# Kernel tuning notes

Hardware: AMD Instinct MI355X
Metric: run time of the kernel (lower is better)

The kernel has to match this reference:

```python
import jax, jax.numpy as jnp
import numpy as np

B = 64           # images
C = 100          # num_categories
LOOP = 3         # LOOP_NUM: max boxes per (image, category)
NB_PER = 150     # boxes per image
N = B * NB_PER   # total boxes
FEAT = 2052      # 2048 backbone feats + 4 bbox coords
OUT = 2048       # gcn_output_shape


def _occ_slots(key):
    """For each element, its occurrence index among equal-valued keys (stable order)."""
    n = key.shape[0]
    order = jnp.argsort(key, stable=True)
    sk = key[order]
    idx = jnp.arange(n)
    is_new = jnp.concatenate([jnp.ones((1,), bool), sk[1:] != sk[:-1]])
    run_start = jax.lax.cummax(jnp.where(is_new, idx, 0))
    pos = idx - run_start
    return jnp.zeros(n, dtype=jnp.int32).at[order].set(pos.astype(jnp.int32))


def setup_inputs() -> dict:
    key = jax.random.key(0)
    ks = jax.random.split(key, 8)
    image_features = jax.random.normal(ks[0], (N, 2048), jnp.float32)
    bbox_list = jax.random.uniform(ks[1], (N, 4), jnp.float32)
    global_features = jax.random.normal(ks[2], (B, C), jnp.float32)
    adj = jax.random.uniform(ks[3], (B, C, C), jnp.float32)
    X = jnp.full((C, C), 1e-6, jnp.float32)                 # nn.Parameter init
    lin_w = jax.random.normal(ks[4], (LOOP,), jnp.float32) * 0.5   # Linear(3,1) weight
    lin_b = jax.random.normal(ks[5], (), jnp.float32) * 0.1        # Linear(3,1) bias
    gc_w = jax.random.normal(ks[6], (FEAT, OUT), jnp.float32) / np.sqrt(FEAT)
    gc_b = jnp.zeros((OUT,), jnp.float32)
    # labels cycle 1..C so each (image, category) appears <= ceil(NB_PER/C)=2 <= LOOP times
    label_list = (jnp.arange(N, dtype=jnp.int32) % C) + 1
    batch = (jnp.arange(N, dtype=jnp.int32) // NB_PER)
    return dict(image_features=image_features, bbox_list=bbox_list,
                global_features=global_features, adj=adj, X=X,
                lin_w=lin_w, lin_b=lin_b, gc_w=gc_w, gc_b=gc_b,
                label_list=label_list, batch=batch)


def reference(image_features, bbox_list, global_features, adj, X,
              lin_w, lin_b, gc_w, gc_b, label_list, batch):
    # full_features = concat(backbone feats, bbox): [N, 2052]
    full = jnp.concatenate([image_features, bbox_list], axis=1)
    cat = label_list - 1
    # occurrence slot of each box within its (image, category) bucket
    slots = _occ_slots(batch.astype(jnp.int64) * C + cat.astype(jnp.int64))
    # scatter-build gcn_input: [B, C, LOOP, 2052]
    gcn_input = jnp.zeros((B, C, LOOP, FEAT), full.dtype).at[batch, cat, slots].set(full)
    # transpose(2,3) then Linear(LOOP -> 1) and squeeze: [B, C, 2052]
    x = jnp.einsum('bcld,l->bcd', gcn_input, lin_w) + lin_b
    # new_adj = X + adj; GraphConvolution: adj @ (x @ W) + b, then leaky_relu
    new_adj = X[None, :, :] + adj
    support = jnp.einsum('bcd,do->bco', x, gc_w)          # [B, C, 2048]
    gcn_out = jax.nn.leaky_relu(jnp.einsum('bcn,bno->bco', new_adj, support) + gc_b)
    # attention aggregate: [B,1,C] @ [B,C,OUT] -> [B,OUT]
    return jnp.einsum('bc,bco->bo', global_features, gcn_out)
```

## Files before the change

kernel.cpp:

```cpp
#include <hip/hip_runtime.h>
#include <stdint.h>

#define BB    64
#define CC    100
#define NBPER 150
#define FEAT  2052
#define KP    2112
#define NOUT  2048
#define MR    6400

typedef __attribute__((ext_vector_type(8))) short   short8;
typedef __attribute__((ext_vector_type(4))) float   floatx4;

__device__ __forceinline__ unsigned short f2bf(float f) {
  unsigned int u = __float_as_uint(f);
  u += 0x7FFFu + ((u >> 16) & 1u);
  return (unsigned short)(u >> 16);
}

__device__ __forceinline__ void async16(const void* g, void* l) {
  __builtin_amdgcn_global_load_lds((__attribute__((address_space(1))) void*)(g),
                                   (__attribute__((address_space(3))) void*)(l),
                                   16, 0, 0);
}

__global__ __launch_bounds__(256) void k_prep(const float* __restrict__ gcw,
                                              unsigned short* __restrict__ gcwT,
                                              const float* __restrict__ imgf,
                                              const float* __restrict__ bbox,
                                              const float* __restrict__ lw,
                                              const float* __restrict__ lb,
                                              const int* __restrict__ labels,
                                              unsigned short* __restrict__ xbf,
                                              const float* __restrict__ X,
                                              const float* __restrict__ adj,
                                              unsigned short* __restrict__ A2p) {
  __shared__ float smf[64 * 65];
  const int bx  = blockIdx.x;
  const int tid = threadIdx.x;

  if (bx < 768) {
    int*   lab  = (int*)smf;
    int*   sidx = lab + NBPER;
    float* swt  = (float*)(sidx + 3 * CC);
    const int bimg = bx / 12;
    const int sl   = bx - bimg * 12;
    if (tid < NBPER) lab[tid] = labels[bimg * NBPER + tid];
    __syncthreads();
    if (tid < CC) {
      int i0 = 0, i1 = 0, i2 = 0, cnt = 0;
      float w0 = 0.f, w1 = 0.f, w2 = 0.f;
      for (int i = 0; i < NBPER; ++i) {
        if (lab[i] == tid + 1) {
          if (cnt == 0)      { i0 = bimg * NBPER + i; w0 = lw[0]; }
          else if (cnt == 1) { i1 = bimg * NBPER + i; w1 = lw[1]; }
          else if (cnt == 2) { i2 = bimg * NBPER + i; w2 = lw[2]; }
          ++cnt;
        }
      }
      sidx[tid * 3] = i0; sidx[tid * 3 + 1] = i1; sidx[tid * 3 + 2] = i2;
      swt[tid * 3] = w0;  swt[tid * 3 + 1] = w1;  swt[tid * 3 + 2] = w2;
    }
    __syncthreads();
    const float bias = lb[0];
    for (int idx = tid; idx < CC * 22; idx += 256) {
      const int cl  = idx / 22;
      const int col = sl * 22 + (idx - cl * 22);
      const int d0  = col * 8;
      const int r   = bimg * CC + cl;
      const int i0 = sidx[cl * 3], i1 = sidx[cl * 3 + 1], i2 = sidx[cl * 3 + 2];
      const float w0 = swt[cl * 3], w1 = swt[cl * 3 + 1], w2 = swt[cl * 3 + 2];
      float v[8];
      if (d0 < 2048) {
        const float4* p0 = (const float4*)(imgf + (size_t)i0 * 2048 + d0);
        const float4* p1 = (const float4*)(imgf + (size_t)i1 * 2048 + d0);
        const float4* p2 = (const float4*)(imgf + (size_t)i2 * 2048 + d0);
        float4 a0 = p0[0], a1 = p0[1];
        float4 b0 = p1[0], b1 = p1[1];
        float4 c0 = p2[0], c1 = p2[1];
        v[0] = bias + w0 * a0.x + w1 * b0.x + w2 * c0.x;
        v[1] = bias + w0 * a0.y + w1 * b0.y + w2 * c0.y;
        v[2] = bias + w0 * a0.z + w1 * b0.z + w2 * c0.z;
        v[3] = bias + w0 * a0.w + w1 * b0.w + w2 * c0.w;
        v[4] = bias + w0 * a1.x + w1 * b1.x + w2 * c1.x;
        v[5] = bias + w0 * a1.y + w1 * b1.y + w2 * c1.y;
        v[6] = bias + w0 * a1.z + w1 * b1.z + w2 * c1.z;
        v[7] = bias + w0 * a1.w + w1 * b1.w + w2 * c1.w;
      } else if (d0 == 2048) {
        float4 u0 = *(const float4*)(bbox + (size_t)i0 * 4);
        float4 u1 = *(const float4*)(bbox + (size_t)i1 * 4);
        float4 u2 = *(const float4*)(bbox + (size_t)i2 * 4);
        v[0] = bias + w0 * u0.x + w1 * u1.x + w2 * u2.x;
        v[1] = bias + w0 * u0.y + w1 * u1.y + w2 * u2.y;
        v[2] = bias + w0 * u0.z + w1 * u1.z + w2 * u2.z;
        v[3] = bias + w0 * u0.w + w1 * u1.w + w2 * u2.w;
        v[4] = 0.f; v[5] = 0.f; v[6] = 0.f; v[7] = 0.f;
      } else {
#pragma unroll
        for (int q = 0; q < 8; ++q) v[q] = 0.f;
      }
      unsigned short o[8] __attribute__((aligned(16)));
#pragma unroll
      for (int q = 0; q < 8; ++q) o[q] = f2bf(v[q]);
      *(uint4*)(xbf + (size_t)r * KP + d0) = *(const uint4*)o;
    }
    return;
  }

  if (bx < 1824) {
    const int t  = bx - 768;
    const int ko = t % 33;
    const int oo = t / 33;
    const int cc = tid & 63, r0 = tid >> 6;
#pragma unroll
    for (int i = 0; i < 16; ++i) {
      const int r = r0 * 16 + i;
      const int k = ko * 64 + r;
      smf[r * 65 + cc] = (k < FEAT) ? gcw[(size_t)k * NOUT + oo * 64 + cc] : 0.f;
    }
    __syncthreads();
    const int ol = tid >> 2;
    const int kq = tid & 3;
    unsigned short buf[16] __attribute__((aligned(16)));
#pragma unroll
    for (int j = 0; j < 16; ++j) buf[j] = f2bf(smf[(kq * 16 + j) * 65 + ol]);
    const size_t base = (size_t)(oo * 64 + ol) * KP + ko * 64 + kq * 16;
    *(uint4*)&gcwT[base]     = *(const uint4*)&buf[0];
    *(uint4*)&gcwT[base + 8] = *(const uint4*)&buf[8];
    return;
  }

  {
    const int b = bx - 1824;
#pragma unroll
    for (int it = 0; it < 16; ++it) {
      const int idx = it * 256 + tid;
      const int c = idx >> 5, ng = idx & 31;
      const int n = ng * 4;
      unsigned short pk[4] __attribute__((aligned(8))) = {0, 0, 0, 0};
      if (c < CC && n < CC) {
        const float4 a4 = *(const float4*)(adj + (size_t)b * (CC * CC) + c * CC + n);
        const float4 x4 = *(const float4*)(X + c * CC + n);
        pk[0] = f2bf(a4.x + x4.x); pk[1] = f2bf(a4.y + x4.y);
        pk[2] = f2bf(a4.z + x4.z); pk[3] = f2bf(a4.w + x4.w);
      }
      *(uint2*)&A2p[((size_t)b * 128 + c) * 128 + n] = *(const uint2*)pk;
    }
  }
}

__global__ __launch_bounds__(256) void k_gemm1(const unsigned short* __restrict__ A,
                                               const unsigned short* __restrict__ Bt,
                                               unsigned short* __restrict__ ST) {
  __shared__ unsigned short shbuf[128 * 132] __attribute__((aligned(16)));
  unsigned short* Asm = shbuf;
  unsigned short* Bsm = shbuf + 8192;
  const int tid  = threadIdx.x;
  const int lane = tid & 63;
  const int w    = tid >> 6;
  const int v    = blockIdx.y * gridDim.x + blockIdx.x;
  const int ncol = (v & 7) * 2 + ((v >> 3) & 1);
  const int mrow = v >> 4;
  const int m0   = mrow * 128;
  const int n0   = ncol * 128;
  const int wm   = (w & 1) * 64;
  const int wn   = (w >> 1) * 64;
  const int srow = lane >> 3;
  const int gk   = (((lane & 7) - srow) & 7) * 8;
  const int quad = lane >> 4;
  const int lrow = lane & 15;
  const int rot  = (lane & 7) * 8;

  floatx4 acc[4][4] = {};

  for (int kb = 0; kb < KP / 64; ++kb) {
    const int k0 = kb * 64;
#pragma unroll
    for (int t = 0; t < 4; ++t) {
      const int chunk = t * 4 + w;
      const int row = chunk * 8 + srow;
      async16(A  + (size_t)(m0 + row) * KP + (k0 + gk), &Asm[chunk * 512]);
      async16(Bt + (size_t)(n0 + row) * KP + (k0 + gk), &Bsm[chunk * 512]);
    }
    __syncthreads();
#pragma unroll
    for (int kp = 0; kp < 2; ++kp) {
      const int koff = (kp * 32 + quad * 8 + rot) & 63;
      short8 af[4], bfr[4];
#pragma unroll
      for (int i = 0; i < 4; ++i)
        af[i]  = *(const short8*)&Asm[(wm + i * 16 + lrow) * 64 + koff];
#pragma unroll
      for (int j = 0; j < 4; ++j)
        bfr[j] = *(const short8*)&Bsm[(wn + j * 16 + lrow) * 64 + koff];
#pragma unroll
      for (int i = 0; i < 4; ++i)
#pragma unroll
        for (int j = 0; j < 4; ++j)
          acc[i][j] = __builtin_amdgcn_mfma_f32_16x16x32_bf16(af[i], bfr[j], acc[i][j], 0, 0, 0);
    }
    __syncthreads();
  }

#pragma unroll
  for (int j = 0; j < 4; ++j) {
    const int ol = wn + j * 16 + lrow;
#pragma unroll
    for (int i = 0; i < 4; ++i) {
#pragma unroll
      for (int rr = 0; rr < 4; ++rr) {
        const int ml = wm + i * 16 + quad * 4 + rr;
        shbuf[ol * 132 + ml] = f2bf(acc[i][j][rr]);
      }
    }
  }
  __syncthreads();
#pragma unroll
  for (int it = 0; it < 32; ++it) {
    const int idx = it * 256 + tid;
    const int o = idx >> 6;
    const int cp = idx & 63;
    const int m = 2 * cp;
    const int r = m0 + m;
    const int b = r / 100;
    const int c = r - b * 100;
    const unsigned int val = *(const unsigned int*)&shbuf[o * 132 + m];
    *(unsigned int*)&ST[((size_t)b * NOUT + n0 + o) * 128 + c] = val;
  }
}

__global__ __launch_bounds__(256) void k_gemm2(const unsigned short* __restrict__ A2p,
                                               const unsigned short* __restrict__ ST,
                                               const float* __restrict__ gf,
                                               const float* __restrict__ gcb,
                                               float* __restrict__ outp) {
  __shared__ unsigned short A2s[128 * 64] __attribute__((aligned(16)));
  __shared__ unsigned short Ssm[128 * 64] __attribute__((aligned(16)));
  __shared__ float gsm[128];
  __shared__ float red[128 * 9];
  const int tid = threadIdx.x;
  const int o0  = blockIdx.x * 128;
  const int b   = blockIdx.y;
  if (tid < 128) gsm[tid] = (tid < CC) ? gf[b * CC + tid] : 0.f;

  const int lane = tid & 63;
  const int w    = tid >> 6;
  const int srow = lane >> 3;
  const int gk   = (((lane & 7) - srow) & 7) * 8;
  const int quad = lane >> 4;
  const int lrow = lane & 15;
  const int rot  = (lane & 7) * 8;
  const int wm   = (w & 1) * 64;
  const int wn   = (w >> 1) * 64;

  floatx4 acc[4][4] = {};

  for (int kb = 0; kb < 2; ++kb) {
    const int k0 = kb * 64;
    __syncthreads();
#pragma unroll
    for (int t = 0; t < 4; ++t) {
      const int chunk = t * 4 + w;
      const int row = chunk * 8 + srow;
      async16(A2p + ((size_t)b * 128 + row) * 128 + k0 + gk, &A2s[chunk * 512]);
      async16(ST + ((size_t)b * NOUT + o0 + row) * 128 + k0 + gk, &Ssm[chunk * 512]);
    }
    __syncthreads();
#pragma unroll
    for (int kp = 0; kp < 2; ++kp) {
      const int koff = (kp * 32 + quad * 8 + rot) & 63;
      short8 af[4], bfr[4];
#pragma unroll
      for (int i = 0; i < 4; ++i)
        af[i]  = *(const short8*)&A2s[(wm + i * 16 + lrow) * 64 + koff];
#pragma unroll
      for (int j = 0; j < 4; ++j)
        bfr[j] = *(const short8*)&Ssm[(wn + j * 16 + lrow) * 64 + koff];
#pragma unroll
      for (int i = 0; i < 4; ++i)
#pragma unroll
        for (int j = 0; j < 4; ++j)
          acc[i][j] = __builtin_amdgcn_mfma_f32_16x16x32_bf16(af[i], bfr[j], acc[i][j], 0, 0, 0);
    }
  }
  __syncthreads();

  const int slot = (w & 1) * 4 + quad;
#pragma unroll
  for (int j = 0; j < 4; ++j) {
    const int ol = wn + j * 16 + lrow;
    const float bias = gcb[o0 + ol];
    float s = 0.f;
#pragma unroll
    for (int i = 0; i < 4; ++i) {
#pragma unroll
      for (int rr = 0; rr < 4; ++rr) {
        const int c = wm + i * 16 + quad * 4 + rr;
        float t = acc[i][j][rr] + bias;
        t = (t > 0.f) ? t : 0.01f * t;
        s += gsm[c] * t;
      }
    }
    red[ol * 9 + slot] = s;
  }
  __syncthreads();
  if (tid < 128) {
    float s = 0.f;
#pragma unroll
    for (int t = 0; t < 8; ++t) s += red[tid * 9 + t];
    outp[(size_t)b * NOUT + o0 + tid] = s;
  }
}

extern "C" void kernel_launch(void* const* d_in, const int* in_sizes, int n_in,
                              void* d_out, int out_size, void* d_ws, size_t ws_size,
                              hipStream_t stream) {
  const float* imgf   = (const float*)d_in[0];
  const float* bbox   = (const float*)d_in[1];
  const float* gfeat  = (const float*)d_in[2];
  const float* adj    = (const float*)d_in[3];
  const float* X      = (const float*)d_in[4];
  const float* lw     = (const float*)d_in[5];
  const float* lb     = (const float*)d_in[6];
  const float* gcw    = (const float*)d_in[7];
  const float* gcb    = (const float*)d_in[8];
  const int*   labels = (const int*)d_in[9];

  char* ws = (char*)d_ws;
  unsigned short* xbf      = (unsigned short*)(ws);
  unsigned short* gcwT     = (unsigned short*)(ws + 27033600);
  unsigned short* supportT = (unsigned short*)(ws + 35684352);
  unsigned short* A2p      = (unsigned short*)(ws + 69238784);
  float*          outp     = (float*)d_out;

  k_prep<<<dim3(1888), dim3(256), 0, stream>>>(gcw, gcwT, imgf, bbox, lw, lb,
                                               labels, xbf, X, adj, A2p);
  k_gemm1<<<dim3(16, 50), dim3(256), 0, stream>>>(xbf, gcwT, supportT);
  k_gemm2<<<dim3(NOUT / 128, BB), dim3(256), 0, stream>>>(A2p, supportT, gfeat, gcb, outp);
}
```

Baseline: 266.2 us.

## Rewrite support GEMM as 256x256-tile, 512-thread double-buffered pipelined kernel

The first GEMM now uses 256x256 output tiles per 512-thread block (8 waves, 128x64 per wave) instead of 128x128 tiles per 256 threads. Global-to-LDS async loads are double-buffered and interleaved with MFMA quarters using explicit vmcnt waits, barriers and s_setprio, so memory traffic overlaps compute rather than stalling on a full sync each k-step. The block-to-tile mapping is also remapped across 200 blocks. The design trades a larger register and LDS footprint and a hand-tuned barrier schedule for more operand reuse and better latency hiding. The epilogue is split into two halves so the transpose fits in the reused LDS.

```diff
diff --git a/kernel.cpp b/kernel.cpp
--- a/kernel.cpp
+++ b/kernel.cpp
@@ -149,83 +149,138 @@
   }
 }
 
-__global__ __launch_bounds__(256) void k_gemm1(const unsigned short* __restrict__ A,
-                                               const unsigned short* __restrict__ Bt,
-                                               unsigned short* __restrict__ ST) {
-  __shared__ unsigned short shbuf[128 * 132] __attribute__((aligned(16)));
-  unsigned short* Asm = shbuf;
-  unsigned short* Bsm = shbuf + 8192;
+__global__ __launch_bounds__(512, 2) void k_gemm1(const unsigned short* __restrict__ Ax,
+                                                  const unsigned short* __restrict__ Bx,
+                                                  unsigned short* __restrict__ ST) {
+  __shared__ unsigned short sh[2][2][16384] __attribute__((aligned(16)));
   const int tid  = threadIdx.x;
   const int lane = tid & 63;
   const int w    = tid >> 6;
-  const int v    = blockIdx.y * gridDim.x + blockIdx.x;
-  const int ncol = (v & 7) * 2 + ((v >> 3) & 1);
-  const int mrow = v >> 4;
-  const int m0   = mrow * 128;
-  const int n0   = ncol * 128;
-  const int wm   = (w & 1) * 64;
-  const int wn   = (w >> 1) * 64;
+  const int wr   = w >> 2;
+  const int wc   = w & 3;
   const int srow = lane >> 3;
   const int gk   = (((lane & 7) - srow) & 7) * 8;
   const int quad = lane >> 4;
   const int lrow = lane & 15;
   const int rot  = (lane & 7) * 8;
-
-  floatx4 acc[4][4] = {};
-
-  for (int kb = 0; kb < KP / 64; ++kb) {
-    const int k0 = kb * 64;
-#pragma unroll
-    for (int t = 0; t < 4; ++t) {
-      const int chunk = t * 4 + w;
-      const int row = chunk * 8 + srow;
-      async16(A  + (size_t)(m0 + row) * KP + (k0 + gk), &Asm[chunk * 512]);
-      async16(Bt + (size_t)(n0 + row) * KP + (k0 + gk), &Bsm[chunk * 512]);
-    }
-    __syncthreads();
-#pragma unroll
-    for (int kp = 0; kp < 2; ++kp) {
-      const int koff = (kp * 32 + quad * 8 + rot) & 63;
-      short8 af[4], bfr[4];
-#pragma unroll
-      for (int i = 0; i < 4; ++i)
-        af[i]  = *(const short8*)&Asm[(wm + i * 16 + lrow) * 64 + koff];
-#pragma unroll
-      for (int j = 0; j < 4; ++j)
-        bfr[j] = *(const short8*)&Bsm[(wn + j * 16 + lrow) * 64 + koff];
-#pragma unroll
-      for (int i = 0; i < 4; ++i)
-#pragma unroll
-        for (int j = 0; j < 4; ++j)
-          acc[i][j] = __builtin_amdgcn_mfma_f32_16x16x32_bf16(af[i], bfr[j], acc[i][j], 0, 0, 0);
-    }
-    __syncthreads();
-  }
-
-#pragma unroll
-  for (int j = 0; j < 4; ++j) {
-    const int ol = wn + j * 16 + lrow;
-#pragma unroll
-    for (int i = 0; i < 4; ++i) {
-#pragma unroll
-      for (int rr = 0; rr < 4; ++rr) {
-        const int ml = wm + i * 16 + quad * 4 + rr;
-        shbuf[ol * 132 + ml] = f2bf(acc[i][j][rr]);
-      }
-    }
-  }
+  const int v    = (blockIdx.x & 7) * 25 + (blockIdx.x >> 3);
+  const int ncol = v / 25;
+  const int mrow = v - ncol * 25;
+  const int m0   = mrow * 256;
+  const int n0   = ncol * 256;
+  const int wm   = wr * 128;
+  const int wn   = wc * 64;
+
+  const unsigned short* pA = Ax + (size_t)(m0 + w * 8 + srow) * KP + gk;
+  const unsigned short* pB = Bx + (size_t)(n0 + w * 8 + srow) * KP + gk;
+
+  floatx4 acc[8][4] = {};
+  short8  afrag[4][2], bfrag[4][2];
+
+#define STG_A(DB, HH, K0) do {                                            \
+    const unsigned short* s_ = pA + (size_t)((HH) * 128) * KP + (K0);     \
+    async16(s_,           &sh[DB][0][(HH) * 8192 + w * 512]);             \
+    async16(s_ + 64 * KP, &sh[DB][0][(HH) * 8192 + (8 + w) * 512]);       \
+  } while (0)
+#define STG_B(DB, HH, K0) do {                                            \
+    const unsigned short* s_ = pB + (size_t)((HH) * 128) * KP + (K0);     \
+    async16(s_,           &sh[DB][1][(HH) * 8192 + w * 512]);             \
+    async16(s_ + 64 * KP, &sh[DB][1][(HH) * 8192 + (8 + w) * 512]);       \
+  } while (0)
+#define RD_B(DB) do {                                                     \
+    _Pragma("unroll") for (int g = 0; g < 4; ++g)                         \
+    _Pragma("unroll") for (int kk = 0; kk < 2; ++kk)                      \
+      bfrag[g][kk] = *(const short8*)&sh[DB][1][(wn + g * 16 + lrow) * 64 \
+                                    + ((kk * 32 + quad * 8 + rot) & 63)]; \
+  } while (0)
+#define RD_A(DB, FO) do {                                                 \
+    _Pragma("unroll") for (int f = 0; f < 4; ++f)                         \
+    _Pragma("unroll") for (int kk = 0; kk < 2; ++kk)                      \
+      afrag[f][kk] = *(const short8*)&sh[DB][0][(wm + ((FO) + f) * 16 + lrow) * 64 \
+                                    + ((kk * 32 + quad * 8 + rot) & 63)]; \
+  } while (0)
+#define MFMA_Q(FO, GO) do {                                               \
+    __builtin_amdgcn_s_setprio(1);                                        \
+    _Pragma("unroll") for (int f = 0; f < 4; ++f)                         \
+    _Pragma("unroll") for (int g = 0; g < 2; ++g)                         \
+    _Pragma("unroll") for (int kk = 0; kk < 2; ++kk)                      \
+      acc[(FO) + f][(GO) + g] = __builtin_amdgcn_mfma_f32_16x16x32_bf16(  \
+          afrag[f][kk], bfrag[(GO) + g][kk], acc[(FO) + f][(GO) + g], 0, 0, 0); \
+    __builtin_amdgcn_s_setprio(0);                                        \
+  } while (0)
+#define BAR __builtin_amdgcn_s_barrier()
+#define VM6 asm volatile("s_waitcnt vmcnt(6)" ::: "memory")
+#define VM0 asm volatile("s_waitcnt vmcnt(0)" ::: "memory")
+
+  STG_B(0, 0, 0);  STG_B(0, 1, 0);  STG_A(0, 0, 0);  STG_A(0, 1, 0);
+  STG_B(1, 0, 64); STG_B(1, 1, 64); STG_A(1, 0, 64);
+  VM6; BAR;
+
+#pragma unroll 1
+  for (int i = 0; i < 15; ++i) {
+    const int kT1 = i * 128 + 64, kT2 = i * 128 + 128, kT3 = i * 128 + 192;
+    RD_B(0); RD_A(0, 0); STG_A(1, 1, kT1); BAR; MFMA_Q(0, 0); BAR;
+    STG_B(0, 0, kT2);                      BAR; MFMA_Q(0, 2); BAR;
+    RD_A(0, 4); STG_B(0, 1, kT2);          BAR; MFMA_Q(4, 0); BAR;
+    STG_A(0, 0, kT2);                      BAR; MFMA_Q(4, 2); VM6; BAR;
+    RD_B(1); RD_A(1, 0); STG_A(0, 1, kT2); BAR; MFMA_Q(0, 0); BAR;
+    STG_B(1, 0, kT3);                      BAR; MFMA_Q(0, 2); BAR;
+    RD_A(1, 4); STG_B(1, 1, kT3);          BAR; MFMA_Q(4, 0); BAR;
+    STG_A(1, 0, kT3);                      BAR; MFMA_Q(4, 2); VM6; BAR;
+  }
+  RD_B(0); RD_A(0, 0); STG_A(1, 1, 1984); BAR; MFMA_Q(0, 0); BAR;
+  STG_B(0, 0, 2048);                      BAR; MFMA_Q(0, 2); BAR;
+  RD_A(0, 4); STG_B(0, 1, 2048);          BAR; MFMA_Q(4, 0); BAR;
+  STG_A(0, 0, 2048);                      BAR; MFMA_Q(4, 2); VM6; BAR;
+  RD_B(1); RD_A(1, 0); STG_A(0, 1, 2048); BAR; MFMA_Q(0, 0); BAR;
+                                          BAR; MFMA_Q(0, 2); BAR;
+  RD_A(1, 4);                             BAR; MFMA_Q(4, 0); BAR;
+                                          BAR; MFMA_Q(4, 2); VM0; BAR;
+  RD_B(0); RD_A(0, 0); MFMA_Q(0, 0); MFMA_Q(0, 2);
+  RD_A(0, 4);          MFMA_Q(4, 0); MFMA_Q(4, 2);
+
+#undef STG_A
+#undef STG_B
+#undef RD_A
+#undef RD_B
+#undef MFMA_Q
+#undef BAR
+#undef VM6
+#undef VM0
+
   __syncthreads();
-#pragma unroll
-  for (int it = 0; it < 32; ++it) {
-    const int idx = it * 256 + tid;
-    const int o = idx >> 6;
-    const int cp = idx & 63;
-    const int m = 2 * cp;
-    const int r = m0 + m;
-    const int b = r / 100;
-    const int c = r - b * 100;
-    const unsigned int val = *(const unsigned int*)&shbuf[o * 132 + m];
-    *(unsigned int*)&ST[((size_t)b * NOUT + n0 + o) * 128 + c] = val;
+  {
+    unsigned short* Tb = &sh[0][0][0];
+#pragma unroll
+    for (int h = 0; h < 2; ++h) {
+      if (h) __syncthreads();
+      if ((wc >> 1) == h) {
+#pragma unroll
+        for (int f = 0; f < 8; ++f) {
+#pragma unroll
+          for (int g = 0; g < 4; ++g) {
+            const int ol = (wc & 1) * 64 + g * 16 + lrow;
+#pragma unroll
+            for (int rr = 0; rr < 4; ++rr) {
+              const int ml = wm + f * 16 + quad * 4 + rr;
+              Tb[ol * 264 + ml] = f2bf(acc[f][g][rr]);
+            }
+          }
+        }
+      }
+      __syncthreads();
+#pragma unroll
+      for (int it = 0; it < 32; ++it) {
+        const int idx = it * 512 + tid;
+        const int o = idx >> 7;
+        const int m = (idx & 127) * 2;
+        const int r = m0 + m;
+        const int b = (r * 5243) >> 19;
+        const int c = r - b * 100;
+        const unsigned int val = *(const unsigned int*)&Tb[o * 264 + m];
+        *(unsigned int*)&ST[((size_t)b * NOUT + n0 + h * 128 + o) * 128 + c] = val;
+      }
+    }
   }
 }
 
@@ -335,6 +390,6 @@
 
   k_prep<<<dim3(1888), dim3(256), 0, stream>>>(gcw, gcwT, imgf, bbox, lw, lb,
                                                labels, xbf, X, adj, A2p);
-  k_gemm1<<<dim3(16, 50), dim3(256), 0, stream>>>(xbf, gcwT, supportT);
+  k_gemm1<<<dim3(200), dim3(512), 0, stream>>>(xbf, gcwT, supportT);
   k_gemm2<<<dim3(NOUT / 128, BB), dim3(256), 0, stream>>>(A2p, supportT, gfeat, gcb, outp);
 }
```

New measurement: 237.3 us. 1.12x faster.
